# Kernel optimization log

Hardware: AMD Instinct MI355X
Metric: run time of the kernel (lower is better)

Reference implementation:

```python
import jax, jax.numpy as jnp
import numpy as np

B, S, D, H = 2, 2048, 1024, 16
DK = D // H

def setup_inputs() -> dict:
    key = jax.random.key(0)
    ks = jax.random.split(key, 8)
    inp = {
        "Q": jax.random.normal(ks[0], (B, S, D), dtype=jnp.float32),
        "K": jax.random.normal(ks[1], (B, S, D), dtype=jnp.float32),
        "V": jax.random.normal(ks[2], (B, S, D), dtype=jnp.float32),
        "mask": jax.random.randint(ks[3], (B, 1, S, S), 0, 2, dtype=jnp.int32),
        # nn.Linear weights, shape [out_features, in_features], no bias
        "Wq": jax.random.normal(ks[4], (D, D), dtype=jnp.float32) / np.sqrt(D),
        "Wk": jax.random.normal(ks[5], (D, D), dtype=jnp.float32) / np.sqrt(D),
        "Wv": jax.random.normal(ks[6], (D, D), dtype=jnp.float32) / np.sqrt(D),
        "Wo": jax.random.normal(ks[7], (D, D), dtype=jnp.float32) / np.sqrt(D),
    }
    return inp

def reference(Q, K, V, mask, Wq, Wk, Wv, Wo):
    b, s, d = Q.shape
    # projections: y = x @ W.T (torch nn.Linear convention)
    q = (Q @ Wq.T).reshape(b, s, H, DK).transpose(0, 2, 1, 3)  # [b,h,s,dk]
    k = (K @ Wk.T).reshape(b, -1, H, DK).transpose(0, 2, 1, 3)
    v = (V @ Wv.T).reshape(b, -1, H, DK).transpose(0, 2, 1, 3)
    score = jnp.einsum("bhqd,bhkd->bhqk", q, k) / jnp.sqrt(jnp.float32(DK))
    # faithful to source: masked positions get value 1e-9 BEFORE softmax
    score = jnp.where(mask == 0, jnp.float32(1e-9), score)
    attn = jax.nn.softmax(score, axis=-1)
    # dropout p=0.1 treated as eval-mode identity
    out = jnp.einsum("bhqk,bhkd->bhqd", attn, v)  # [b,h,s,dk]
    out = out.transpose(0, 2, 1, 3).reshape(b, s, d)
    return out @ Wo.T
```

## Files before the change

kernel.cpp:

```cpp
#include <hip/hip_runtime.h>

typedef unsigned short u16;
typedef unsigned char  u8;
typedef unsigned long long u64;
typedef __attribute__((ext_vector_type(8))) short bf16x8;
typedef __attribute__((ext_vector_type(4))) float f32x4;

constexpr int B_  = 2;
constexpr int S_  = 2048;
constexpr int D_  = 1024;
constexpr int H_  = 16;
constexpr int DK_ = 64;
constexpr int NROW = B_ * S_;
constexpr size_t QSZ  = (size_t)B_ * H_ * S_ * DK_;
constexpr size_t XBSZ = (size_t)NROW * D_;
constexpr size_t WBSZ = (size_t)D_ * D_;
constexpr size_t MSZ  = (size_t)B_ * S_ * S_;
constexpr size_t MPKB = MSZ / 8;

__device__ __forceinline__ u16 f2bf(float f) {
    union { float f; unsigned u; } c; c.f = f;
    unsigned r = c.u + 0x7fffu + ((c.u >> 16) & 1u);
    return (u16)(r >> 16);
}
__device__ __forceinline__ unsigned pack2(float a, float b) {
    return (unsigned)f2bf(a) | ((unsigned)f2bf(b) << 16);
}
__device__ __forceinline__ unsigned cvt_pk_bf16(float a, float b) {
    unsigned r;
    asm("v_cvt_pk_bf16_f32 %0, %1, %2" : "=v"(r) : "v"(a), "v"(b));
    return r;
}

__device__ __forceinline__ void gl_lds16(const u16* g, u16* l) {
    __builtin_amdgcn_global_load_lds(
        (const __attribute__((address_space(1))) void*)g,
        (__attribute__((address_space(3))) void*)l, 16, 0, 0);
}

__global__ __launch_bounds__(256)
void cvt7m(const float* __restrict__ s0, const float* __restrict__ s1,
           const float* __restrict__ s2, const float* __restrict__ s3,
           const float* __restrict__ s4, const float* __restrict__ s5,
           const float* __restrict__ s6, const int* __restrict__ mk,
           u16* __restrict__ d0, u16* __restrict__ d1, u16* __restrict__ d2,
           u16* __restrict__ d3, u16* __restrict__ d4, u16* __restrict__ d5,
           u16* __restrict__ d6, u8* __restrict__ mp)
{
    constexpr size_t XT = 3 * XBSZ;
    constexpr int NCF = (int)((3 * XBSZ + 4 * WBSZ) / 2048);
    constexpr int NCM = (int)(MSZ / 2048);

    for (int c = blockIdx.x; c < NCF + NCM; c += gridDim.x) {
        if (c < NCF) {
            const size_t base = (size_t)c * 2048;
            const float* s; u16* d; size_t off;
            if (base < XT) {
                const int a = (int)(base >> 22);
                off = base & (XBSZ - 1);
                s = (a == 0) ? s0 : (a == 1) ? s1 : s2;
                d = (a == 0) ? d0 : (a == 1) ? d1 : d2;
            } else {
                const size_t r = base - XT;
                const int a = (int)(r >> 20);
                off = r & (WBSZ - 1);
                s = (a == 0) ? s3 : (a == 1) ? s4 : (a == 2) ? s5 : s6;
                d = (a == 0) ? d3 : (a == 1) ? d4 : (a == 2) ? d5 : d6;
            }
            const size_t e = off + (size_t)threadIdx.x * 8;
            const float4 x0 = *(const float4*)(s + e);
            const float4 x1 = *(const float4*)(s + e + 4);
            uint4 p;
            p.x = pack2(x0.x, x0.y); p.y = pack2(x0.z, x0.w);
            p.z = pack2(x1.x, x1.y); p.w = pack2(x1.z, x1.w);
            *(uint4*)(d + e) = p;
        } else {
            const size_t e = (size_t)(c - NCF) * 2048 + (size_t)threadIdx.x * 8;
            const int4 x0 = *(const int4*)(mk + e);
            const int4 x1 = *(const int4*)(mk + e + 4);
            unsigned bv = (unsigned)(x0.x != 0)        | ((unsigned)(x0.y != 0) << 1)
                        | ((unsigned)(x0.z != 0) << 2) | ((unsigned)(x0.w != 0) << 3)
                        | ((unsigned)(x1.x != 0) << 4) | ((unsigned)(x1.y != 0) << 5)
                        | ((unsigned)(x1.z != 0) << 6) | ((unsigned)(x1.w != 0) << 7);
            mp[e >> 3] = (u8)bv;
        }
    }
}

__global__ __launch_bounds__(256, 3)
void qkv_gemm(const u16* __restrict__ Xq, const u16* __restrict__ Xk,
              const u16* __restrict__ Xv,
              const u16* __restrict__ Wq, const u16* __restrict__ Wk,
              const u16* __restrict__ Wv,
              u16* __restrict__ Yq, u16* __restrict__ Yk, u16* __restrict__ Yv)
{
    __shared__ u16 As[2 * 128 * 32];
    __shared__ u16 Bs[2 * 128 * 32];

    const int z = blockIdx.z;
    const u16* X = (z == 0) ? Xq : (z == 1) ? Xk : Xv;
    const u16* W = (z == 0) ? Wq : (z == 1) ? Wk : Wv;
    u16*       Y = (z == 0) ? Yq : (z == 1) ? Yk : Yv;
    const float osc = (z == 0) ? 0.125f : 1.0f;

    const int tid  = threadIdx.x;
    const int lane = tid & 63;
    const int w    = tid >> 6;
    const int quad = lane >> 4;
    const int lq   = lane & 15;
    const int wm   = (w & 1) << 6;
    const int wn   = (w >> 1) << 6;

    const int bid2 = (int)(blockIdx.x + (blockIdx.y << 5));
    const int swz2 = (bid2 & 7) * 32 + (bid2 >> 3);
    const int m0 = (swz2 & 31) << 7;
    const int n0 = (swz2 >> 5) << 7;

    const int srow = tid >> 2;
    const int scol = (tid & 3) << 3;
    const u16* ga0 = X + (size_t)(m0 + srow) * D_ + scol;
    const u16* ga1 = ga0 + (size_t)64 * D_;
    const u16* gb0 = W + (size_t)(n0 + srow) * D_ + scol;
    const u16* gb1 = gb0 + (size_t)64 * D_;

    u16* la0 = As + (size_t)w * 512;
    u16* la1 = As + 2048 + (size_t)w * 512;
    u16* lb0 = Bs + (size_t)w * 512;
    u16* lb1 = Bs + 2048 + (size_t)w * 512;

    f32x4 acc[4][4];
#pragma unroll
    for (int i = 0; i < 4; ++i)
#pragma unroll
        for (int j = 0; j < 4; ++j) acc[i][j] = (f32x4){0.f, 0.f, 0.f, 0.f};

    for (int kt = 0; kt < D_; kt += 64) {
        __syncthreads();
        gl_lds16(ga0 + kt, la0);
        gl_lds16(ga1 + kt, la1);
        gl_lds16(gb0 + kt, lb0);
        gl_lds16(gb1 + kt, lb1);
        gl_lds16(ga0 + kt + 32, la0 + 4096);
        gl_lds16(ga1 + kt + 32, la1 + 4096);
        gl_lds16(gb0 + kt + 32, lb0 + 4096);
        gl_lds16(gb1 + kt + 32, lb1 + 4096);
        __syncthreads();

#pragma unroll
        for (int kk = 0; kk < 2; ++kk) {
            bf16x8 af[4], bf[4];
#pragma unroll
            for (int t = 0; t < 4; ++t) {
                af[t] = *(const bf16x8*)&As[(kk << 12) + (size_t)(wm + (t << 4) + lq) * 32 + (quad << 3)];
                bf[t] = *(const bf16x8*)&Bs[(kk << 12) + (size_t)(wn + (t << 4) + lq) * 32 + (quad << 3)];
            }
#pragma unroll
            for (int i = 0; i < 4; ++i)
#pragma unroll
                for (int j = 0; j < 4; ++j)
                    acc[i][j] = __builtin_amdgcn_mfma_f32_16x16x32_bf16(
                        af[i], bf[j], acc[i][j], 0, 0, 0);
        }
    }

#pragma unroll
    for (int i = 0; i < 4; ++i)
#pragma unroll
        for (int j = 0; j < 4; ++j)
#pragma unroll
            for (int r = 0; r < 4; ++r) {
                const int grow = m0 + wm + (i << 4) + (quad << 2) + r;
                const int of   = n0 + wn + (j << 4) + lq;
                const int b = grow >> 11, s = grow & (S_ - 1);
                const int h = of >> 6,    dk = of & 63;
                Y[(((size_t)(b * H_ + h)) * S_ + s) * DK_ + dk] =
                    f2bf(acc[i][j][r] * osc);
            }
}

__global__ __launch_bounds__(256, 4)
void out_gemm(const u16* __restrict__ X, const u16* __restrict__ W,
              float* __restrict__ Y)
{
    __shared__ u16 As[2 * 64 * 32];
    __shared__ u16 Bs[2 * 64 * 32];

    const int tid  = threadIdx.x;
    const int lane = tid & 63;
    const int w    = tid >> 6;
    const int quad = lane >> 4;
    const int lq   = lane & 15;
    const int wm   = (w & 1) << 5;
    const int wn   = (w >> 1) << 5;

    const int bid2 = (int)(blockIdx.x + (blockIdx.y << 6));
    const int swz2 = (bid2 & 7) * 128 + (bid2 >> 3);
    const int m0 = (swz2 & 63) << 6;
    const int n0 = (swz2 >> 6) << 6;

    const int srow = tid >> 2;
    const int scol = (tid & 3) << 3;
    const u16* ga0 = X + (size_t)(m0 + srow) * D_ + scol;
    const u16* gb0 = W + (size_t)(n0 + srow) * D_ + scol;

    u16* la0 = As + (size_t)w * 512;
    u16* lb0 = Bs + (size_t)w * 512;

    f32x4 acc[2][2];
#pragma unroll
    for (int i = 0; i < 2; ++i)
#pragma unroll
        for (int j = 0; j < 2; ++j) acc[i][j] = (f32x4){0.f, 0.f, 0.f, 0.f};

    for (int kt = 0; kt < D_; kt += 64) {
        __syncthreads();
        gl_lds16(ga0 + kt, la0);
        gl_lds16(gb0 + kt, lb0);
        gl_lds16(ga0 + kt + 32, la0 + 2048);
        gl_lds16(gb0 + kt + 32, lb0 + 2048);
        __syncthreads();

#pragma unroll
        for (int kk = 0; kk < 2; ++kk) {
            bf16x8 af[2], bf[2];
#pragma unroll
            for (int t = 0; t < 2; ++t) {
                af[t] = *(const bf16x8*)&As[(kk << 11) + (size_t)(wm + (t << 4) + lq) * 32 + (quad << 3)];
                bf[t] = *(const bf16x8*)&Bs[(kk << 11) + (size_t)(wn + (t << 4) + lq) * 32 + (quad << 3)];
            }
#pragma unroll
            for (int i = 0; i < 2; ++i)
#pragma unroll
                for (int j = 0; j < 2; ++j)
                    acc[i][j] = __builtin_amdgcn_mfma_f32_16x16x32_bf16(
                        af[i], bf[j], acc[i][j], 0, 0, 0);
        }
    }

#pragma unroll
    for (int i = 0; i < 2; ++i)
#pragma unroll
        for (int j = 0; j < 2; ++j)
#pragma unroll
            for (int r = 0; r < 4; ++r) {
                const int grow = m0 + wm + (i << 4) + (quad << 2) + r;
                const int gcol = n0 + wn + (j << 4) + lq;
                Y[(size_t)grow * D_ + gcol] = acc[i][j][r];
            }
}

constexpr int AP = 72;

__global__ __launch_bounds__(256, 2)
void attn_mfma8(const u16* __restrict__ qb, const u16* __restrict__ kb,
                const u16* __restrict__ vb, const u8* __restrict__ mpk,
                u16* __restrict__ ctx)
{
    __shared__ u16 Qs[128][AP];
    __shared__ u16 Ks[64][AP];
    __shared__ u16 Vt[64][AP];
    __shared__ u16 Ps[128][AP];

    const int tid  = threadIdx.x;
    const int lane = tid & 63;
    const int w    = tid >> 6;
    const int quad = lane >> 4;
    const int lq   = lane & 15;
    const int w32  = w << 5;

    const int bid = (int)(blockIdx.x + gridDim.x * (blockIdx.y + gridDim.y * blockIdx.z));
    const int swz = (bid & 7) * 64 + (bid >> 3);
    const int q0 = (swz & 15) << 7;
    const int h  = (swz >> 4) & 15;
    const int b  = swz >> 8;

    const u16* qbh = qb + (((size_t)b * H_ + h) * S_ + q0) * DK_;
    const u16* kbh = kb + ((size_t)b * H_ + h) * S_ * DK_;
    const u16* vbh = vb + ((size_t)b * H_ + h) * S_ * DK_;

    {
        const int r = tid >> 1, c = (tid & 1) << 5;
#pragma unroll
        for (int u = 0; u < 4; ++u)
            *(uint4*)&Qs[r][c + (u << 3)] =
                *(const uint4*)&qbh[(size_t)r * DK_ + c + (u << 3)];
    }
    __syncthreads();
    bf16x8 aQ[2][2];
#pragma unroll
    for (int i = 0; i < 2; ++i) {
        aQ[i][0] = *(const bf16x8*)&Qs[w32 + (i << 4) + lq][quad << 3];
        aQ[i][1] = *(const bf16x8*)&Qs[w32 + (i << 4) + lq][32 + (quad << 3)];
    }

    f32x4 O[2][4];
    float lsum[2][4];
#pragma unroll
    for (int i = 0; i < 2; ++i)
#pragma unroll
        for (int t = 0; t < 4; ++t) O[i][t] = (f32x4){0.f, 0.f, 0.f, 0.f};
#pragma unroll
    for (int i = 0; i < 2; ++i)
#pragma unroll
        for (int r = 0; r < 4; ++r) lsum[i][r] = 0.f;

    const int ksr = tid >> 2, ksc = (tid & 3) << 4;
    const int vc  = tid & 15;
    const int vs  = (tid >> 4) & 1;
    const int vk0 = vc + (vs << 5);
    const int vdg = tid >> 5;
    const int vcol = (vc << 2) + (vs << 1);

    uint4 kr0, kr1, vr0, vr1;
    {
        kr0 = *(const uint4*)&kbh[(size_t)ksr * DK_ + ksc];
        kr1 = *(const uint4*)&kbh[(size_t)ksr * DK_ + ksc + 8];
        vr0 = *(const uint4*)&vbh[(size_t)vk0 * DK_ + (vdg << 3)];
        vr1 = *(const uint4*)&vbh[(size_t)(vk0 + 16) * DK_ + (vdg << 3)];
    }

    const int qrow0 = q0 + w32 + (quad << 2);
    const u8* mrow = mpk + (size_t)b * S_ * (S_ / 8) + (size_t)qrow0 * (S_ / 8);

    for (int k0 = 0; k0 < S_; k0 += 64) {
        u64 mw[2][4];
#pragma unroll
        for (int i = 0; i < 2; ++i)
#pragma unroll
            for (int r = 0; r < 4; ++r)
                mw[i][r] = *(const u64*)&mrow[(size_t)((i << 4) + r) * (S_ / 8) + (k0 >> 3)];

        __syncthreads();
        {
            *(uint4*)&Ks[ksr][ksc]     = kr0;
            *(uint4*)&Ks[ksr][ksc + 8] = kr1;
            const u16* a0 = (const u16*)&vr0;
            const u16* a1 = (const u16*)&vr1;
#pragma unroll
            for (int i = 0; i < 8; ++i)
                *(ushort2*)&Vt[(vdg << 3) + i][vcol] = (ushort2){a0[i], a1[i]};
        }
        __syncthreads();

        if (k0 + 64 < S_) {
            const size_t kb0 = (size_t)(k0 + 64 + ksr) * DK_ + ksc;
            kr0 = *(const uint4*)&kbh[kb0];
            kr1 = *(const uint4*)&kbh[kb0 + 8];
            const size_t vb0 = (size_t)(k0 + 64 + vk0) * DK_ + (vdg << 3);
            vr0 = *(const uint4*)&vbh[vb0];
            vr1 = *(const uint4*)&vbh[vb0 + (size_t)16 * DK_];
        }

        f32x4 st[2][4];
#pragma unroll
        for (int t = 0; t < 4; ++t) {
            const bf16x8 b0 = *(const bf16x8*)&Ks[(t << 4) + lq][quad << 3];
            const bf16x8 b1 = *(const bf16x8*)&Ks[(t << 4) + lq][32 + (quad << 3)];
#pragma unroll
            for (int i = 0; i < 2; ++i) {
                f32x4 c = {0.f, 0.f, 0.f, 0.f};
                c = __builtin_amdgcn_mfma_f32_16x16x32_bf16(aQ[i][0], b0, c, 0, 0, 0);
                c = __builtin_amdgcn_mfma_f32_16x16x32_bf16(aQ[i][1], b1, c, 0, 0, 0);
                st[i][t] = c;
            }
        }

#pragma unroll
        for (int i = 0; i < 2; ++i)
#pragma unroll
            for (int r = 0; r < 4; ++r) {
                const unsigned lo = (unsigned)mw[i][r];
                const unsigned hi = (unsigned)(mw[i][r] >> 32);
                float p0 = __expf(st[i][0][r]);
                float p1 = __expf(st[i][1][r]);
                float p2 = __expf(st[i][2][r]);
                float p3 = __expf(st[i][3][r]);
                p0 = ((lo >> lq) & 1u) ? p0 : 1.0f;
                p1 = ((lo >> (lq + 16)) & 1u) ? p1 : 1.0f;
                p2 = ((hi >> lq) & 1u) ? p2 : 1.0f;
                p3 = ((hi >> (lq + 16)) & 1u) ? p3 : 1.0f;
                lsum[i][r] += (p0 + p1) + (p2 + p3);
                uint2 pw;
                pw.x = cvt_pk_bf16(p0, p1);
                pw.y = cvt_pk_bf16(p2, p3);
                *(uint2*)&Ps[w32 + (i << 4) + (quad << 2) + r][lq << 2] = pw;
            }

        bf16x8 aP[2][2];
#pragma unroll
        for (int i = 0; i < 2; ++i) {
            aP[i][0] = *(const bf16x8*)&Ps[w32 + (i << 4) + lq][quad << 3];
            aP[i][1] = *(const bf16x8*)&Ps[w32 + (i << 4) + lq][32 + (quad << 3)];
        }
#pragma unroll
        for (int t = 0; t < 4; ++t) {
            const bf16x8 b0 = *(const bf16x8*)&Vt[(t << 4) + lq][quad << 3];
            const bf16x8 b1 = *(const bf16x8*)&Vt[(t << 4) + lq][32 + (quad << 3)];
#pragma unroll
            for (int i = 0; i < 2; ++i) {
                O[i][t] = __builtin_amdgcn_mfma_f32_16x16x32_bf16(aP[i][0], b0, O[i][t], 0, 0, 0);
                O[i][t] = __builtin_amdgcn_mfma_f32_16x16x32_bf16(aP[i][1], b1, O[i][t], 0, 0, 0);
            }
        }
    }

#pragma unroll
    for (int i = 0; i < 2; ++i)
#pragma unroll
        for (int r = 0; r < 4; ++r) {
#pragma unroll
            for (int off = 1; off < 16; off <<= 1)
                lsum[i][r] += __shfl_xor(lsum[i][r], off);
            lsum[i][r] = 1.0f / lsum[i][r];
        }

#pragma unroll
    for (int i = 0; i < 2; ++i)
#pragma unroll
        for (int t = 0; t < 4; ++t)
#pragma unroll
            for (int r = 0; r < 4; ++r) {
                const int row = qrow0 + (i << 4) + r;
                ctx[((size_t)b * S_ + row) * D_ + (h << 6) + (t << 4) + lq] =
                    f2bf(O[i][t][r] * lsum[i][r]);
            }
}

extern "C" void kernel_launch(void* const* d_in, const int* in_sizes, int n_in,
                              void* d_out, int out_size, void* d_ws, size_t ws_size,
                              hipStream_t stream)
{
    const float* Q    = (const float*)d_in[0];
    const float* K    = (const float*)d_in[1];
    const float* V    = (const float*)d_in[2];
    const int*   mask = (const int*)d_in[3];
    const float* Wq   = (const float*)d_in[4];
    const float* Wk   = (const float*)d_in[5];
    const float* Wv   = (const float*)d_in[6];
    const float* Wo   = (const float*)d_in[7];
    float* out = (float*)d_out;

    u16* xqb = (u16*)d_ws;
    u16* xkb = xqb + XBSZ;
    u16* xvb = xqb + 2 * XBSZ;
    u16* wqb = xqb + 3 * XBSZ;
    u16* wkb = wqb + WBSZ;
    u16* wvb = wqb + 2 * WBSZ;
    u16* wob = wqb + 3 * WBSZ;
    u16* qw  = wqb + 4 * WBSZ;
    u16* kw  = qw + QSZ;
    u16* vw  = qw + 2 * QSZ;
    u8*  mpk = (u8*)(qw + 3 * QSZ);
    u16* cx  = xqb;

    hipLaunchKernelGGL(cvt7m, dim3(2048), dim3(256), 0, stream,
                       Q, K, V, Wq, Wk, Wv, Wo, mask,
                       xqb, xkb, xvb, wqb, wkb, wvb, wob, mpk);
    hipLaunchKernelGGL(qkv_gemm, dim3(NROW / 128, D_ / 128, 3), dim3(256), 0, stream,
                       xqb, xkb, xvb, wqb, wkb, wvb, qw, kw, vw);
    hipLaunchKernelGGL(attn_mfma8, dim3(S_ / 128, H_, B_), dim3(256), 0, stream,
                       qw, kw, vw, mpk, cx);
    hipLaunchKernelGGL(out_gemm, dim3(NROW / 64, D_ / 64), dim3(256), 0, stream,
                       cx, wob, out);
}
```

Measured before the change: 252.1 us.

## Double-buffer LDS in both GEMMs and K/V tiles in attention

Both projection GEMMs now issue the global-to-LDS loads for the next 32-wide K slice into a second buffer while the current slice is being multiplied. This cuts the per-step synchronisation to one barrier per slice. The attention kernel double-buffers the K and V shared tiles, and reuses the Q staging buffer for P to save LDS. It also moves the mask word loads after the barrier so they overlap with compute. A single barrier per iteration with ping-pong buffers relies on correct ordering, and the extra LDS per block may affect occupancy.

```diff
diff --git a/kernel.cpp b/kernel.cpp
--- a/kernel.cpp
+++ b/kernel.cpp
@@ -88,11 +88,11 @@
 }
 
 __global__ __launch_bounds__(256, 3)
-void qkv_gemm(const u16* __restrict__ Xq, const u16* __restrict__ Xk,
-              const u16* __restrict__ Xv,
-              const u16* __restrict__ Wq, const u16* __restrict__ Wk,
-              const u16* __restrict__ Wv,
-              u16* __restrict__ Yq, u16* __restrict__ Yk, u16* __restrict__ Yv)
+void qkv_gemm2(const u16* __restrict__ Xq, const u16* __restrict__ Xk,
+               const u16* __restrict__ Xv,
+               const u16* __restrict__ Wq, const u16* __restrict__ Wk,
+               const u16* __restrict__ Wv,
+               u16* __restrict__ Yq, u16* __restrict__ Yk, u16* __restrict__ Yv)
 {
     __shared__ u16 As[2 * 128 * 32];
     __shared__ u16 Bs[2 * 128 * 32];
@@ -123,10 +123,7 @@
     const u16* gb0 = W + (size_t)(n0 + srow) * D_ + scol;
     const u16* gb1 = gb0 + (size_t)64 * D_;
 
-    u16* la0 = As + (size_t)w * 512;
-    u16* la1 = As + 2048 + (size_t)w * 512;
-    u16* lb0 = Bs + (size_t)w * 512;
-    u16* lb1 = Bs + 2048 + (size_t)w * 512;
+    const int wof = w << 9;
 
     f32x4 acc[4][4];
 #pragma unroll
@@ -134,33 +131,35 @@
 #pragma unroll
         for (int j = 0; j < 4; ++j) acc[i][j] = (f32x4){0.f, 0.f, 0.f, 0.f};
 
-    for (int kt = 0; kt < D_; kt += 64) {
+    gl_lds16(ga0, As + wof);
+    gl_lds16(ga1, As + 2048 + wof);
+    gl_lds16(gb0, Bs + wof);
+    gl_lds16(gb1, Bs + 2048 + wof);
+
+    for (int kt = 0; kt < D_; kt += 32) {
+        const int bi = (kt >> 5) & 1;
+        const int bo = bi << 12;
         __syncthreads();
-        gl_lds16(ga0 + kt, la0);
-        gl_lds16(ga1 + kt, la1);
-        gl_lds16(gb0 + kt, lb0);
-        gl_lds16(gb1 + kt, lb1);
-        gl_lds16(ga0 + kt + 32, la0 + 4096);
-        gl_lds16(ga1 + kt + 32, la1 + 4096);
-        gl_lds16(gb0 + kt + 32, lb0 + 4096);
-        gl_lds16(gb1 + kt + 32, lb1 + 4096);
-        __syncthreads();
-
-#pragma unroll
-        for (int kk = 0; kk < 2; ++kk) {
-            bf16x8 af[4], bf[4];
-#pragma unroll
-            for (int t = 0; t < 4; ++t) {
-                af[t] = *(const bf16x8*)&As[(kk << 12) + (size_t)(wm + (t << 4) + lq) * 32 + (quad << 3)];
-                bf[t] = *(const bf16x8*)&Bs[(kk << 12) + (size_t)(wn + (t << 4) + lq) * 32 + (quad << 3)];
-            }
-#pragma unroll
-            for (int i = 0; i < 4; ++i)
-#pragma unroll
-                for (int j = 0; j < 4; ++j)
-                    acc[i][j] = __builtin_amdgcn_mfma_f32_16x16x32_bf16(
-                        af[i], bf[j], acc[i][j], 0, 0, 0);
-        }
+        if (kt + 32 < D_) {
+            const int no = (bo ^ 4096);
+            gl_lds16(ga0 + kt + 32, As + no + wof);
+            gl_lds16(ga1 + kt + 32, As + no + 2048 + wof);
+            gl_lds16(gb0 + kt + 32, Bs + no + wof);
+            gl_lds16(gb1 + kt + 32, Bs + no + 2048 + wof);
+        }
+
+        bf16x8 af[4], bf[4];
+#pragma unroll
+        for (int t = 0; t < 4; ++t) {
+            af[t] = *(const bf16x8*)&As[bo + (size_t)(wm + (t << 4) + lq) * 32 + (quad << 3)];
+            bf[t] = *(const bf16x8*)&Bs[bo + (size_t)(wn + (t << 4) + lq) * 32 + (quad << 3)];
+        }
+#pragma unroll
+        for (int i = 0; i < 4; ++i)
+#pragma unroll
+            for (int j = 0; j < 4; ++j)
+                acc[i][j] = __builtin_amdgcn_mfma_f32_16x16x32_bf16(
+                    af[i], bf[j], acc[i][j], 0, 0, 0);
     }
 
 #pragma unroll
@@ -179,8 +178,8 @@
 }
 
 __global__ __launch_bounds__(256, 4)
-void out_gemm(const u16* __restrict__ X, const u16* __restrict__ W,
-              float* __restrict__ Y)
+void out_gemm2(const u16* __restrict__ X, const u16* __restrict__ W,
+               float* __restrict__ Y)
 {
     __shared__ u16 As[2 * 64 * 32];
     __shared__ u16 Bs[2 * 64 * 32];
@@ -203,8 +202,7 @@
     const u16* ga0 = X + (size_t)(m0 + srow) * D_ + scol;
     const u16* gb0 = W + (size_t)(n0 + srow) * D_ + scol;
 
-    u16* la0 = As + (size_t)w * 512;
-    u16* lb0 = Bs + (size_t)w * 512;
+    const int wof = w << 9;
 
     f32x4 acc[2][2];
 #pragma unroll
@@ -212,29 +210,31 @@
 #pragma unroll
         for (int j = 0; j < 2; ++j) acc[i][j] = (f32x4){0.f, 0.f, 0.f, 0.f};
 
-    for (int kt = 0; kt < D_; kt += 64) {
+    gl_lds16(ga0, As + wof);
+    gl_lds16(gb0, Bs + wof);
+
+    for (int kt = 0; kt < D_; kt += 32) {
+        const int bi = (kt >> 5) & 1;
+        const int bo = bi << 11;
         __syncthreads();
-        gl_lds16(ga0 + kt, la0);
-        gl_lds16(gb0 + kt, lb0);
-        gl_lds16(ga0 + kt + 32, la0 + 2048);
-        gl_lds16(gb0 + kt + 32, lb0 + 2048);
-        __syncthreads();
-
-#pragma unroll
-        for (int kk = 0; kk < 2; ++kk) {
-            bf16x8 af[2], bf[2];
-#pragma unroll
-            for (int t = 0; t < 2; ++t) {
-                af[t] = *(const bf16x8*)&As[(kk << 11) + (size_t)(wm + (t << 4) + lq) * 32 + (quad << 3)];
-                bf[t] = *(const bf16x8*)&Bs[(kk << 11) + (size_t)(wn + (t << 4) + lq) * 32 + (quad << 3)];
-            }
-#pragma unroll
-            for (int i = 0; i < 2; ++i)
-#pragma unroll
-                for (int j = 0; j < 2; ++j)
-                    acc[i][j] = __builtin_amdgcn_mfma_f32_16x16x32_bf16(
-                        af[i], bf[j], acc[i][j], 0, 0, 0);
-        }
+        if (kt + 32 < D_) {
+            const int no = (bo ^ 2048);
+            gl_lds16(ga0 + kt + 32, As + no + wof);
+            gl_lds16(gb0 + kt + 32, Bs + no + wof);
+        }
+
+        bf16x8 af[2], bf[2];
+#pragma unroll
+        for (int t = 0; t < 2; ++t) {
+            af[t] = *(const bf16x8*)&As[bo + (size_t)(wm + (t << 4) + lq) * 32 + (quad << 3)];
+            bf[t] = *(const bf16x8*)&Bs[bo + (size_t)(wn + (t << 4) + lq) * 32 + (quad << 3)];
+        }
+#pragma unroll
+        for (int i = 0; i < 2; ++i)
+#pragma unroll
+            for (int j = 0; j < 2; ++j)
+                acc[i][j] = __builtin_amdgcn_mfma_f32_16x16x32_bf16(
+                    af[i], bf[j], acc[i][j], 0, 0, 0);
     }
 
 #pragma unroll
@@ -252,14 +252,13 @@
 constexpr int AP = 72;
 
 __global__ __launch_bounds__(256, 2)
-void attn_mfma8(const u16* __restrict__ qb, const u16* __restrict__ kb,
-                const u16* __restrict__ vb, const u8* __restrict__ mpk,
-                u16* __restrict__ ctx)
+void attn_mfma11(const u16* __restrict__ qb, const u16* __restrict__ kb,
+                 const u16* __restrict__ vb, const u8* __restrict__ mpk,
+                 u16* __restrict__ ctx)
 {
-    __shared__ u16 Qs[128][AP];
-    __shared__ u16 Ks[64][AP];
-    __shared__ u16 Vt[64][AP];
-    __shared__ u16 Ps[128][AP];
+    __shared__ u16 QPs[128][AP];
+    __shared__ u16 Ks[2][64][AP];
+    __shared__ u16 Vt[2][64][AP];
 
     const int tid  = threadIdx.x;
     const int lane = tid & 63;
@@ -282,15 +281,15 @@
         const int r = tid >> 1, c = (tid & 1) << 5;
 #pragma unroll
         for (int u = 0; u < 4; ++u)
-            *(uint4*)&Qs[r][c + (u << 3)] =
+            *(uint4*)&QPs[r][c + (u << 3)] =
                 *(const uint4*)&qbh[(size_t)r * DK_ + c + (u << 3)];
     }
     __syncthreads();
     bf16x8 aQ[2][2];
 #pragma unroll
     for (int i = 0; i < 2; ++i) {
-        aQ[i][0] = *(const bf16x8*)&Qs[w32 + (i << 4) + lq][quad << 3];
-        aQ[i][1] = *(const bf16x8*)&Qs[w32 + (i << 4) + lq][32 + (quad << 3)];
+        aQ[i][0] = *(const bf16x8*)&QPs[w32 + (i << 4) + lq][quad << 3];
+        aQ[i][1] = *(const bf16x8*)&QPs[w32 + (i << 4) + lq][32 + (quad << 3)];
     }
 
     f32x4 O[2][4];
@@ -323,22 +322,16 @@
     const u8* mrow = mpk + (size_t)b * S_ * (S_ / 8) + (size_t)qrow0 * (S_ / 8);
 
     for (int k0 = 0; k0 < S_; k0 += 64) {
-        u64 mw[2][4];
-#pragma unroll
-        for (int i = 0; i < 2; ++i)
-#pragma unroll
-            for (int r = 0; r < 4; ++r)
-                mw[i][r] = *(const u64*)&mrow[(size_t)((i << 4) + r) * (S_ / 8) + (k0 >> 3)];
-
-        __syncthreads();
+        const int bi = (k0 >> 6) & 1;
+
         {
-            *(uint4*)&Ks[ksr][ksc]     = kr0;
-            *(uint4*)&Ks[ksr][ksc + 8] = kr1;
+            *(uint4*)&Ks[bi][ksr][ksc]     = kr0;
+            *(uint4*)&Ks[bi][ksr][ksc + 8] = kr1;
             const u16* a0 = (const u16*)&vr0;
             const u16* a1 = (const u16*)&vr1;
 #pragma unroll
             for (int i = 0; i < 8; ++i)
-                *(ushort2*)&Vt[(vdg << 3) + i][vcol] = (ushort2){a0[i], a1[i]};
+                *(ushort2*)&Vt[bi][(vdg << 3) + i][vcol] = (ushort2){a0[i], a1[i]};
         }
         __syncthreads();
 
@@ -351,11 +344,18 @@
             vr1 = *(const uint4*)&vbh[vb0 + (size_t)16 * DK_];
         }
 
+        u64 mw[2][4];
+#pragma unroll
+        for (int i = 0; i < 2; ++i)
+#pragma unroll
+            for (int r = 0; r < 4; ++r)
+                mw[i][r] = *(const u64*)&mrow[(size_t)((i << 4) + r) * (S_ / 8) + (k0 >> 3)];
+
         f32x4 st[2][4];
 #pragma unroll
         for (int t = 0; t < 4; ++t) {
-            const bf16x8 b0 = *(const bf16x8*)&Ks[(t << 4) + lq][quad << 3];
-            const bf16x8 b1 = *(const bf16x8*)&Ks[(t << 4) + lq][32 + (quad << 3)];
+            const bf16x8 b0 = *(const bf16x8*)&Ks[bi][(t << 4) + lq][quad << 3];
+            const bf16x8 b1 = *(const bf16x8*)&Ks[bi][(t << 4) + lq][32 + (quad << 3)];
 #pragma unroll
             for (int i = 0; i < 2; ++i) {
                 f32x4 c = {0.f, 0.f, 0.f, 0.f};
@@ -383,19 +383,19 @@
                 uint2 pw;
                 pw.x = cvt_pk_bf16(p0, p1);
                 pw.y = cvt_pk_bf16(p2, p3);
-                *(uint2*)&Ps[w32 + (i << 4) + (quad << 2) + r][lq << 2] = pw;
+                *(uint2*)&QPs[w32 + (i << 4) + (quad << 2) + r][lq << 2] = pw;
             }
 
         bf16x8 aP[2][2];
 #pragma unroll
         for (int i = 0; i < 2; ++i) {
-            aP[i][0] = *(const bf16x8*)&Ps[w32 + (i << 4) + lq][quad << 3];
-            aP[i][1] = *(const bf16x8*)&Ps[w32 + (i << 4) + lq][32 + (quad << 3)];
+            aP[i][0] = *(const bf16x8*)&QPs[w32 + (i << 4) + lq][quad << 3];
+            aP[i][1] = *(const bf16x8*)&QPs[w32 + (i << 4) + lq][32 + (quad << 3)];
         }
 #pragma unroll
         for (int t = 0; t < 4; ++t) {
-            const bf16x8 b0 = *(const bf16x8*)&Vt[(t << 4) + lq][quad << 3];
-            const bf16x8 b1 = *(const bf16x8*)&Vt[(t << 4) + lq][32 + (quad << 3)];
+            const bf16x8 b0 = *(const bf16x8*)&Vt[bi][(t << 4) + lq][quad << 3];
+            const bf16x8 b1 = *(const bf16x8*)&Vt[bi][(t << 4) + lq][32 + (quad << 3)];
 #pragma unroll
             for (int i = 0; i < 2; ++i) {
                 O[i][t] = __builtin_amdgcn_mfma_f32_16x16x32_bf16(aP[i][0], b0, O[i][t], 0, 0, 0);
@@ -456,10 +456,10 @@
     hipLaunchKernelGGL(cvt7m, dim3(2048), dim3(256), 0, stream,
                        Q, K, V, Wq, Wk, Wv, Wo, mask,
                        xqb, xkb, xvb, wqb, wkb, wvb, wob, mpk);
-    hipLaunchKernelGGL(qkv_gemm, dim3(NROW / 128, D_ / 128, 3), dim3(256), 0, stream,
+    hipLaunchKernelGGL(qkv_gemm2, dim3(NROW / 128, D_ / 128, 3), dim3(256), 0, stream,
                        xqb, xkb, xvb, wqb, wkb, wvb, qw, kw, vw);
-    hipLaunchKernelGGL(attn_mfma8, dim3(S_ / 128, H_, B_), dim3(256), 0, stream,
+    hipLaunchKernelGGL(attn_mfma11, dim3(S_ / 128, H_, B_), dim3(256), 0, stream,
                        qw, kw, vw, mpk, cx);
-    hipLaunchKernelGGL(out_gemm, dim3(NROW / 64, D_ / 64), dim3(256), 0, stream,
+    hipLaunchKernelGGL(out_gemm2, dim3(NROW / 64, D_ / 64), dim3(256), 0, stream,
                        cx, wob, out);
 }
```

Result: no change. 254.4 us (median of 2 runs) (+0.9%).
